# Performance work log

Hardware: AMD Instinct MI355X
Metric: run time of the kernel (lower is better)

Reference implementation:

```python
import jax, jax.numpy as jnp
import numpy as np

NUM_HEADS = 16
HEAD_SIZE = 64
MAX_POS = 2048  # config.max_position_embeddings


def setup_inputs() -> dict:
    key = jax.random.key(0)
    ks = jax.random.split(key, 8)
    B, Lq, Lk, D = 4, 1024, 2048, 1024
    s = 1.0 / np.sqrt(D)
    return {
        "hidden_states": jax.random.normal(ks[0], (B, Lk, D), jnp.float32),
        "query_hidden_states": jax.random.normal(ks[1], (B, Lq, D), jnp.float32),
        "attention_mask": jnp.zeros((B, 1, 1, Lk), jnp.float32),
        "Wq": jax.random.normal(ks[2], (D, D), jnp.float32) * s,
        "bq": jnp.zeros((D,), jnp.float32),
        "Wk": jax.random.normal(ks[3], (D, D), jnp.float32) * s,
        "bk": jnp.zeros((D,), jnp.float32),
        "Wv": jax.random.normal(ks[4], (D, D), jnp.float32) * s,
        "bv": jnp.zeros((D,), jnp.float32),
        "dist_emb": jax.random.normal(ks[5], (2 * MAX_POS - 1, HEAD_SIZE), jnp.float32) * 0.02,
    }


def _split_heads(x):
    # [B, L, H*Dh] -> [B, H, L, Dh]
    B, L, _ = x.shape
    return x.reshape(B, L, NUM_HEADS, HEAD_SIZE).transpose(0, 2, 1, 3)


def reference(hidden_states, query_hidden_states, attention_mask, Wq, bq, Wk, bk, Wv, bv, dist_emb):
    # Linear projections (torch Linear: x @ W.T + b)
    q = _split_heads(query_hidden_states @ Wq.T + bq)   # [B,H,Lq,Dh]
    k = _split_heads(hidden_states @ Wk.T + bk)          # [B,H,Lk,Dh]
    v = _split_heads(hidden_states @ Wv.T + bv)          # [B,H,Lk,Dh]

    scores = jnp.einsum('bhld,bhrd->bhlr', q, k)         # [B,H,Lq,Lk]

    # relative_key_query positional scores
    Lq, Lk = q.shape[2], k.shape[2]
    distance = jnp.arange(Lq)[:, None] - jnp.arange(Lk)[None, :]
    pe = dist_emb[distance + MAX_POS - 1]                # [Lq,Lk,Dh]
    scores = scores + jnp.einsum('bhld,lrd->bhlr', q, pe) + jnp.einsum('bhrd,lrd->bhlr', k, pe)

    scores = scores / np.sqrt(HEAD_SIZE) + attention_mask
    probs = jax.nn.softmax(scores, axis=-1)              # dropout p=0 (eval)
    ctx = jnp.einsum('bhlr,bhrd->bhld', probs, v)        # [B,H,Lq,Dh]
    B = ctx.shape[0]
    return ctx.transpose(0, 2, 1, 3).reshape(B, Lq, NUM_HEADS * HEAD_SIZE)
```

## Files before the change

### kernel.cpp

```cpp
#include <hip/hip_runtime.h>
#include <hip/hip_bf16.h>

#define B_   4
#define H_   16
#define LQ   1024
#define LK   2048
#define D_   1024
#define DH   64

typedef __attribute__((ext_vector_type(8))) short  short8;
typedef __attribute__((ext_vector_type(4))) float  float4_;
typedef __attribute__((ext_vector_type(4))) unsigned int uint4_;

static __device__ __forceinline__ float bf2f(unsigned short u) {
    unsigned int x = ((unsigned int)u) << 16;
    return __builtin_bit_cast(float, x);
}
static __device__ __forceinline__ unsigned short f2bf(float f) {
    unsigned int x = __builtin_bit_cast(unsigned int, f);
    unsigned int lsb = (x >> 16) & 1u;
    x += 0x7fffu + lsb;
    return (unsigned short)(x >> 16);
}
static __device__ __forceinline__ unsigned int pack2(float a, float b) {
    __hip_bfloat162 h = __float22bfloat162_rn(make_float2(a, b));
    unsigned int r;
    __builtin_memcpy(&r, &h, 4);
    return r;
}

#define MFMA(a, b, c) __builtin_amdgcn_mfma_f32_16x16x32_bf16((a), (b), (c), 0, 0, 0)

#define GLOAD_LDS16(g, l) __builtin_amdgcn_global_load_lds( \
    (const __attribute__((address_space(1))) unsigned int*)(const void*)(g), \
    (__attribute__((address_space(3))) unsigned int*)(void*)(l), 16, 0, 0)

__global__ __launch_bounds__(256) void conv_kernel(
    const float* __restrict__ Wq, const float* __restrict__ Wk,
    const float* __restrict__ Wv, const float* __restrict__ Eg,
    const float* __restrict__ Xq, const float* __restrict__ Xk,
    unsigned short* __restrict__ cWq, unsigned short* __restrict__ cWk,
    unsigned short* __restrict__ cWv, unsigned short* __restrict__ cEb,
    unsigned short* __restrict__ cXq, unsigned short* __restrict__ cXk)
{
    int bid = blockIdx.x;
    const float* src; unsigned short* dst; int nch;
    if (bid < 512)       { src = Wq; dst = cWq;              nch = 131072;  }
    else if (bid < 1024) { src = Wk; dst = cWk; bid -= 512;  nch = 131072;  }
    else if (bid < 1536) { src = Wv; dst = cWv; bid -= 1024; nch = 131072;  }
    else if (bid < 1664) { src = Eg; dst = cEb; bid -= 1536; nch = 32760;   }
    else if (bid < 3712) { src = Xq; dst = cXq; bid -= 1664; nch = 524288;  }
    else                 { src = Xk; dst = cXk; bid -= 3712; nch = 1048576; }
    int ch = bid * 256 + threadIdx.x;
    if (ch >= nch) return;
    const float* s = src + (size_t)ch * 8;
    float4_ v0 = *(const float4_*)s, v1 = *(const float4_*)(s + 4);
    uint4_ o;
    o[0] = pack2(v0[0], v0[1]); o[1] = pack2(v0[2], v0[3]);
    o[2] = pack2(v1[0], v1[1]); o[3] = pack2(v1[2], v1[3]);
    *(uint4_*)(dst + (size_t)ch * 8) = o;
}

__global__ __launch_bounds__(256) void proj_kernel(
    const unsigned short* __restrict__ Xq, const unsigned short* __restrict__ Xk,
    const unsigned short* __restrict__ Wq, const float* __restrict__ bq,
    const unsigned short* __restrict__ Wk, const float* __restrict__ bk,
    const unsigned short* __restrict__ Wv, const float* __restrict__ bv,
    unsigned short* __restrict__ Qh, unsigned short* __restrict__ Kh,
    unsigned short* __restrict__ VT)
{
    __shared__ short smem[32768];
    short* A0 = smem;
    short* B0 = smem + 8192;
    short* A1 = smem + 16384;
    short* B1 = smem + 24576;
    short* Cs = smem;

    int bid = blockIdx.x;
    int which, tm, tn;
    const unsigned short *X; const float* bias; const unsigned short* W;
    if (bid < 256)      { which = 0; int t = bid;       tm = t >> 3; tn = t & 7; X = Xq; W = Wq; bias = bq; }
    else if (bid < 768) { which = 1; int t = bid - 256; tm = t >> 3; tn = t & 7; X = Xk; W = Wk; bias = bk; }
    else                { which = 2; int t = bid - 768; tm = t >> 3; tn = t & 7; X = Xk; W = Wv; bias = bv; }

    int tid  = threadIdx.x;
    int wave = tid >> 6, lane = tid & 63;
    int wr = (wave >> 1) * 64, wc = (wave & 1) * 64;
    int m0 = tm * 128, n0 = tn * 128;

    float4_ acc[4][4];
    for (int a = 0; a < 4; ++a) for (int c = 0; c < 4; ++c) acc[a][c] = (float4_)0.0f;

    int rl = lane >> 3;
    int chs = (lane & 7) ^ rl;
    const unsigned short* Asrc = X + (size_t)(m0 + wave * 32 + rl) * D_ + (chs << 3);
    const unsigned short* Bsrc = W + (size_t)(n0 + wave * 32 + rl) * D_ + (chs << 3);

    int lrow = lane & 15, lk8 = (lane >> 4) * 8;
    int swz = lane & 7;

    auto stage = [&](short* Ad, short* Bd, int kt) {
        int k0 = kt * 64;
        #pragma unroll
        for (int c = 0; c < 4; ++c) {
            GLOAD_LDS16(Asrc + (size_t)(c * 8) * D_ + k0, &Ad[(wave * 32 + c * 8) * 64]);
            GLOAD_LDS16(Bsrc + (size_t)(c * 8) * D_ + k0, &Bd[(wave * 32 + c * 8) * 64]);
        }
    };
    auto compute = [&](const short* Aa, const short* Bb) {
        #pragma unroll
        for (int kk = 0; kk < 64; kk += 32) {
            int cgrp = (kk + lk8) >> 3;
            int coff = ((cgrp ^ swz) << 3);
            short8 af[4], bfr[4];
            #pragma unroll
            for (int rt = 0; rt < 4; ++rt)
                af[rt]  = *(const short8*)(&Aa[(wr + rt * 16 + lrow) * 64 + coff]);
            #pragma unroll
            for (int ct = 0; ct < 4; ++ct)
                bfr[ct] = *(const short8*)(&Bb[(wc + ct * 16 + lrow) * 64 + coff]);
            #pragma unroll
            for (int rt = 0; rt < 4; ++rt)
                #pragma unroll
                for (int ct = 0; ct < 4; ++ct)
                    acc[rt][ct] = MFMA(af[rt], bfr[ct], acc[rt][ct]);
        }
    };

    stage(A0, B0, 0);
    __syncthreads();
    for (int kt = 0; kt < 16; kt += 2) {
        if (kt + 1 < 16) stage(A1, B1, kt + 1);
        compute(A0, B0);
        __syncthreads();
        if (kt + 2 < 16) stage(A0, B0, kt + 2);
        compute(A1, B1);
        __syncthreads();
    }

    int lrow4 = (lane >> 4) * 4, lcol = lane & 15;
    if (which < 2) {
        int lsh = (which == 0) ? 10 : 11;
        int Lm1 = (1 << lsh) - 1;
        unsigned short* dst = (which == 0) ? Qh : Kh;
        for (int rt = 0; rt < 4; ++rt)
            for (int ct = 0; ct < 4; ++ct)
                for (int i = 0; i < 4; ++i) {
                    int m = m0 + wr + rt * 16 + lrow4 + i;
                    int n = n0 + wc + ct * 16 + lcol;
                    float v = acc[rt][ct][i] + bias[n];
                    int b = m >> lsh, s = m & Lm1;
                    int h = n >> 6, d = n & 63;
                    dst[((size_t)((b * H_ + h) << lsh) + (size_t)s) * DH + d] = f2bf(v);
                }
    } else {
        for (int rt = 0; rt < 4; ++rt)
            for (int ct = 0; ct < 4; ++ct)
                for (int i = 0; i < 4; ++i) {
                    int rl2 = wr + rt * 16 + lrow4 + i;
                    int cl  = wc + ct * 16 + lcol;
                    float v = acc[rt][ct][i] + bias[n0 + cl];
                    Cs[cl * 136 + rl2] = (short)f2bf(v);
                }
        __syncthreads();
        int b = m0 >> 11, r0 = m0 & 2047;
        int c = tid >> 1, half = tid & 1;
        int n = n0 + c, h = n >> 6, d = n & 63;
        unsigned short* dstp = VT + ((size_t)(b * H_ + h) * DH + d) * LK + r0 + half * 64;
        for (int j = 0; j < 8; ++j) {
            uint4_ v = *(const uint4_*)(&Cs[c * 136 + half * 64 + j * 8]);
            *(uint4_*)(dstp + j * 8) = v;
        }
    }
}

__global__ __launch_bounds__(256, 2) void attn_kernel(
    const unsigned short* __restrict__ Qh, const unsigned short* __restrict__ Kh,
    const unsigned short* __restrict__ VT, const unsigned short* __restrict__ Eb,
    const float* __restrict__ mask, float* __restrict__ out)
{
    __shared__ short smem[31360];
    short* Qs  = smem;
    short* Ks  = smem;
    short* VTs = smem + 4608;
    short* Es  = smem + 9216;
    short* Ps  = smem + 18432;
    unsigned int* Gqk = (unsigned int*)(smem + 23040);
    short* Gs  = smem + 23040;

    int bid = blockIdx.x;
    int l0 = (bid & 15) * 64;
    int bh = bid >> 4;
    int b  = bh >> 4, h = bh & 15;
    int tid = threadIdx.x, wave = tid >> 6, lane = tid & 63;
    int lr = lane & 15, lk8 = (lane >> 4) * 8, lr4 = (lane >> 4) * 4;

    for (int i = 0; i < 2; ++i) {
        int idx = tid + 256 * i, row = idx >> 3, g = (idx & 7) * 8;
        *(uint4_*)(&Qs[row * 72 + g]) =
            *(const uint4_*)(Qh + ((size_t)(bh * LQ + l0 + row)) * DH + g);
    }
    __syncthreads();
    short8 aq0 = *(const short8*)(&Qs[(wave * 16 + lr) * 72 + lk8]);
    short8 aq1 = *(const short8*)(&Qs[(wave * 16 + lr) * 72 + 32 + lk8]);

    float m_i[4], l_i[4];
    float4_ Oacc[4];
    for (int i = 0; i < 4; ++i) { m_i[i] = -1e30f; l_i[i] = 0.f; Oacc[i] = (float4_)0.f; }

    const unsigned short* Kbase = Kh + (size_t)bh * LK * DH;
    const unsigned short* Vbase = VT + (size_t)bh * DH * LK;

    int srow = tid >> 3;
    int sg   = (tid & 7) * 8;

    uint4_ kr0, kr1, vr0, vr1, er0, er1, er2, er3;
    auto load_tiles = [&](int it2) {
        int r0_ = it2 * 64, jb_ = l0 - r0_ + 1984;
        kr0 = *(const uint4_*)(Kbase + (size_t)(r0_ + srow) * DH + sg);
        kr1 = *(const uint4_*)(Kbase + (size_t)(r0_ + srow + 32) * DH + sg);
        vr0 = *(const uint4_*)(Vbase + (size_t)srow * LK + r0_ + sg);
        vr1 = *(const uint4_*)(Vbase + (size_t)(srow + 32) * LK + r0_ + sg);
        er0 = *(const uint4_*)(Eb + (size_t)(jb_ + srow) * DH + sg);
        er1 = *(const uint4_*)(Eb + (size_t)(jb_ + srow + 32) * DH + sg);
        er2 = *(const uint4_*)(Eb + (size_t)(jb_ + srow + 64) * DH + sg);
        er3 = *(const uint4_*)(Eb + (size_t)(jb_ + srow + 96) * DH + sg);
    };
    load_tiles(0);

    for (int it = 0; it < 32; ++it) {
        int r0 = it * 64;

        __syncthreads();
        *(uint4_*)(&Ks[srow * 72 + sg])         = kr0;
        *(uint4_*)(&Ks[(srow + 32) * 72 + sg])  = kr1;
        *(uint4_*)(&VTs[srow * 72 + sg])        = vr0;
        *(uint4_*)(&VTs[(srow + 32) * 72 + sg]) = vr1;
        *(uint4_*)(&Es[srow * 72 + sg])         = er0;
        *(uint4_*)(&Es[(srow + 32) * 72 + sg])  = er1;
        *(uint4_*)(&Es[(srow + 64) * 72 + sg])  = er2;
        *(uint4_*)(&Es[(srow + 96) * 72 + sg])  = er3;
        __syncthreads();
        if (it < 31) load_tiles(it + 1);

        float4_ Sacc[4];
        for (int c = 0; c < 4; ++c) {
            short8 b0 = *(const short8*)(&Ks[(c * 16 + lr) * 72 + lk8]);
            short8 b1 = *(const short8*)(&Ks[(c * 16 + lr) * 72 + 32 + lk8]);
            float4_ s = (float4_)0.f;
            s = MFMA(aq0, b0, s);
            s = MFMA(aq1, b1, s);
            Sacc[c] = s;
        }

        short8 ak0 = *(const short8*)(&Ks[(wave * 16 + lr) * 72 + lk8]);
        short8 ak1 = *(const short8*)(&Ks[(wave * 16 + lr) * 72 + 32 + lk8]);
        unsigned int gqp[5][2], gkp[5][2];
        for (int tt = 0; tt < 5; ++tt) {
            int tqi = wave + tt;
            short8 e0 = *(const short8*)(&Es[(tqi * 16 + lr) * 72 + lk8]);
            short8 e1 = *(const short8*)(&Es[(tqi * 16 + lr) * 72 + 32 + lk8]);
            float4_ g = (float4_)0.f;
            g = MFMA(aq0, e0, g); g = MFMA(aq1, e1, g);
            gqp[tt][0] = pack2(g[0], g[1]); gqp[tt][1] = pack2(g[2], g[3]);
            int tk = (3 - wave) + tt;
            short8 f0 = *(const short8*)(&Es[(tk * 16 + lr) * 72 + lk8]);
            short8 f1 = *(const short8*)(&Es[(tk * 16 + lr) * 72 + 32 + lk8]);
            float4_ gg = (float4_)0.f;
            gg = MFMA(ak0, f0, gg); gg = MFMA(ak1, f1, gg);
            gkp[tt][0] = pack2(gg[0], gg[1]); gkp[tt][1] = pack2(gg[2], gg[3]);
        }

        for (int tt = 0; tt < 5; ++tt) {
            int uq = (wave + tt) * 16 + lr;
            int uk = (3 - wave + tt) * 16 + lr;
            for (int i = 0; i < 4; ++i) {
                int row = wave * 16 + lr4 + i;
                unsigned int wq32 = gqp[tt][i >> 1], wk32 = gkp[tt][i >> 1];
                unsigned short vq = (unsigned short)((i & 1) ? (wq32 >> 16) : (wq32 & 0xffff));
                unsigned short vk = (unsigned short)((i & 1) ? (wk32 >> 16) : (wk32 & 0xffff));
                int tr = row - uq + 63;
                if ((unsigned)tr < 64u)
                    Gs[(row * 65 + tr) * 2] = (short)vq;
                int tl = uk + row - 63;
                if ((unsigned)tl < 64u)
                    Gs[(tl * 65 + row) * 2 + 1] = (short)vk;
            }
        }
        __syncthreads();

        float mk[4];
        for (int c = 0; c < 4; ++c) mk[c] = mask[b * LK + r0 + c * 16 + lr];
        for (int i = 0; i < 4; ++i) {
            int tl = wave * 16 + lr4 + i;
            const unsigned int* gr = Gqk + tl * 65 + lr;
            unsigned int gva[4];
            gva[0] = gr[0]; gva[1] = gr[16]; gva[2] = gr[32]; gva[3] = gr[48];
            float scv[4], mx = -1e30f;
            #pragma unroll
            for (int c = 0; c < 4; ++c) {
                float sq = bf2f((unsigned short)(gva[c] & 0xffff));
                float sk = bf2f((unsigned short)(gva[c] >> 16));
                float sc = (Sacc[c][i] + sq + sk) * 0.125f + mk[c];
                scv[c] = sc;
                mx = fmaxf(mx, sc);
            }
            for (int off = 1; off < 16; off <<= 1) mx = fmaxf(mx, __shfl_xor(mx, off, 64));
            float mnew = fmaxf(m_i[i], mx);
            float alpha = __expf(m_i[i] - mnew);
            m_i[i] = mnew;
            float e0 = __expf(scv[0] - mnew), e1 = __expf(scv[1] - mnew);
            float e2 = __expf(scv[2] - mnew), e3 = __expf(scv[3] - mnew);
            unsigned int p01 = pack2(e0, e1), p23 = pack2(e2, e3);
            float rs = bf2f((unsigned short)(p01 & 0xffff)) + bf2f((unsigned short)(p01 >> 16))
                     + bf2f((unsigned short)(p23 & 0xffff)) + bf2f((unsigned short)(p23 >> 16));
            for (int off = 1; off < 16; off <<= 1) rs += __shfl_xor(rs, off, 64);
            l_i[i] = l_i[i] * alpha + rs;
            for (int nt = 0; nt < 4; ++nt) Oacc[nt][i] *= alpha;
            short* Pr = Ps + tl * 72;
            Pr[ 0 + lr] = (short)(unsigned short)(p01 & 0xffff);
            Pr[16 + lr] = (short)(unsigned short)(p01 >> 16);
            Pr[32 + lr] = (short)(unsigned short)(p23 & 0xffff);
            Pr[48 + lr] = (short)(unsigned short)(p23 >> 16);
        }
        const short* Pa = Ps + (wave * 16 + lr) * 72;
        short8 ap0 = *(const short8*)(Pa + lk8);
        short8 ap1 = *(const short8*)(Pa + 32 + lk8);
        for (int nt = 0; nt < 4; ++nt) {
            short8 v0 = *(const short8*)(&VTs[(nt * 16 + lr) * 72 + lk8]);
            short8 v1 = *(const short8*)(&VTs[(nt * 16 + lr) * 72 + 32 + lk8]);
            Oacc[nt] = MFMA(ap0, v0, Oacc[nt]);
            Oacc[nt] = MFMA(ap1, v1, Oacc[nt]);
        }
    }

    for (int nt = 0; nt < 4; ++nt)
        for (int i = 0; i < 4; ++i) {
            int row = l0 + wave * 16 + lr4 + i;
            int col = h * 64 + nt * 16 + lr;
            out[(size_t)(b * LQ + row) * D_ + col] = Oacc[nt][i] / l_i[i];
        }
}

extern "C" void kernel_launch(void* const* d_in, const int* in_sizes, int n_in,
                              void* d_out, int out_size, void* d_ws, size_t ws_size,
                              hipStream_t stream) {
    (void)in_sizes; (void)n_in; (void)out_size; (void)ws_size;
    const float* Xk   = (const float*)d_in[0];
    const float* Xq   = (const float*)d_in[1];
    const float* mask = (const float*)d_in[2];
    const float* Wq   = (const float*)d_in[3];
    const float* bq   = (const float*)d_in[4];
    const float* Wk   = (const float*)d_in[5];
    const float* bk   = (const float*)d_in[6];
    const float* Wv   = (const float*)d_in[7];
    const float* bv   = (const float*)d_in[8];
    const float* Eg   = (const float*)d_in[9];

    unsigned short* Qh  = (unsigned short*)d_ws;
    unsigned short* Kh  = Qh  + (size_t)4194304;
    unsigned short* VT  = Kh  + (size_t)8388608;
    unsigned short* cWq = VT  + (size_t)8388608;
    unsigned short* cWk = cWq + (size_t)1048576;
    unsigned short* cWv = cWk + (size_t)1048576;
    unsigned short* cEb = cWv + (size_t)1048576;
    unsigned short* cXq = cEb + (size_t)262144;
    unsigned short* cXk = (unsigned short*)d_out;
    float* o = (float*)d_out;

    conv_kernel<<<7808, 256, 0, stream>>>(Wq, Wk, Wv, Eg, Xq, Xk,
                                          cWq, cWk, cWv, cEb, cXq, cXk);
    proj_kernel<<<1280, 256, 0, stream>>>(cXq, cXk, cWq, bq, cWk, bk, cWv, bv, Qh, Kh, VT);
    attn_kernel<<<1024, 256, 0, stream>>>(Qh, Kh, VT, cEb, mask, o);
}
```

Baseline: 425.3 us.

## Keep sliding positional-embedding window in registers and use DPP row reductions

The attention loop no longer stages the 128-row distance-embedding window through shared memory each iteration. Each lane holds the 8 E fragments in registers, and only the 4 newly needed tiles are loaded per step, using an xor-indexed double buffer across a two-iteration unrolled loop. The per-wave E MFMAs are restructured to skip tiles a wave does not need, and the K fragment is reused from the score loop. The 16-lane max and sum reductions switch from shfl_xor to DPP moves. Shared memory use drops, at the cost of many more VGPRs and strided direct global loads for E.

```diff
diff --git a/kernel.cpp b/kernel.cpp
--- a/kernel.cpp
+++ b/kernel.cpp
@@ -27,6 +27,12 @@
     unsigned int r;
     __builtin_memcpy(&r, &h, 4);
     return r;
+}
+template<int CTRL>
+static __device__ __forceinline__ float dppmv(float x) {
+    int i = __builtin_bit_cast(int, x);
+    int r = __builtin_amdgcn_update_dpp(i, i, CTRL, 0xf, 0xf, false);
+    return __builtin_bit_cast(float, r);
 }
 
 #define MFMA(a, b, c) __builtin_amdgcn_mfma_f32_16x16x32_bf16((a), (b), (c), 0, 0, 0)
@@ -179,14 +185,13 @@
     const unsigned short* __restrict__ VT, const unsigned short* __restrict__ Eb,
     const float* __restrict__ mask, float* __restrict__ out)
 {
-    __shared__ short smem[31360];
+    __shared__ short smem[22144];
     short* Qs  = smem;
     short* Ks  = smem;
     short* VTs = smem + 4608;
-    short* Es  = smem + 9216;
-    short* Ps  = smem + 18432;
-    unsigned int* Gqk = (unsigned int*)(smem + 23040);
-    short* Gs  = smem + 23040;
+    short* Ps  = smem + 9216;
+    unsigned int* Gqk = (unsigned int*)(smem + 13824);
+    short* Gs  = smem + 13824;
 
     int bid = blockIdx.x;
     int l0 = (bid & 15) * 64;
@@ -214,21 +219,31 @@
     int srow = tid >> 3;
     int sg   = (tid & 7) * 8;
 
-    uint4_ kr0, kr1, vr0, vr1, er0, er1, er2, er3;
-    auto load_tiles = [&](int it2) {
-        int r0_ = it2 * 64, jb_ = l0 - r0_ + 1984;
+    uint4_ kr0, kr1, vr0, vr1;
+    auto load_kv = [&](int nit) {
+        int r0_ = nit * 64;
         kr0 = *(const uint4_*)(Kbase + (size_t)(r0_ + srow) * DH + sg);
         kr1 = *(const uint4_*)(Kbase + (size_t)(r0_ + srow + 32) * DH + sg);
         vr0 = *(const uint4_*)(Vbase + (size_t)srow * LK + r0_ + sg);
         vr1 = *(const uint4_*)(Vbase + (size_t)(srow + 32) * LK + r0_ + sg);
-        er0 = *(const uint4_*)(Eb + (size_t)(jb_ + srow) * DH + sg);
-        er1 = *(const uint4_*)(Eb + (size_t)(jb_ + srow + 32) * DH + sg);
-        er2 = *(const uint4_*)(Eb + (size_t)(jb_ + srow + 64) * DH + sg);
-        er3 = *(const uint4_*)(Eb + (size_t)(jb_ + srow + 96) * DH + sg);
     };
-    load_tiles(0);
-
-    for (int it = 0; it < 32; ++it) {
+    load_kv(0);
+
+    short8 ef[8][2];
+    {
+        const unsigned short* ep = Eb + (size_t)(l0 + 1984 + lr) * DH + lk8;
+        #pragma unroll
+        for (int t = 0; t < 8; ++t) {
+            ef[t][0] = *(const short8*)(ep + (size_t)t * 16 * DH);
+            ef[t][1] = *(const short8*)(ep + (size_t)t * 16 * DH + 32);
+        }
+    }
+
+    for (int it2 = 0; it2 < 32; it2 += 2) {
+      #pragma unroll
+      for (int sub = 0; sub < 2; ++sub) {
+        const int it = it2 + sub;
+        const int p4 = sub * 4;
         int r0 = it * 64;
 
         __syncthreads();
@@ -236,14 +251,12 @@
         *(uint4_*)(&Ks[(srow + 32) * 72 + sg])  = kr1;
         *(uint4_*)(&VTs[srow * 72 + sg])        = vr0;
         *(uint4_*)(&VTs[(srow + 32) * 72 + sg]) = vr1;
-        *(uint4_*)(&Es[srow * 72 + sg])         = er0;
-        *(uint4_*)(&Es[(srow + 32) * 72 + sg])  = er1;
-        *(uint4_*)(&Es[(srow + 64) * 72 + sg])  = er2;
-        *(uint4_*)(&Es[(srow + 96) * 72 + sg])  = er3;
-        __syncthreads();
-        if (it < 31) load_tiles(it + 1);
-
+        __syncthreads();
+        if (it < 31) load_kv(it + 1);
+
+        short8 ak0, ak1;
         float4_ Sacc[4];
+        #pragma unroll
         for (int c = 0; c < 4; ++c) {
             short8 b0 = *(const short8*)(&Ks[(c * 16 + lr) * 72 + lk8]);
             short8 b1 = *(const short8*)(&Ks[(c * 16 + lr) * 72 + 32 + lk8]);
@@ -251,46 +264,60 @@
             s = MFMA(aq0, b0, s);
             s = MFMA(aq1, b1, s);
             Sacc[c] = s;
-        }
-
-        short8 ak0 = *(const short8*)(&Ks[(wave * 16 + lr) * 72 + lk8]);
-        short8 ak1 = *(const short8*)(&Ks[(wave * 16 + lr) * 72 + 32 + lk8]);
-        unsigned int gqp[5][2], gkp[5][2];
-        for (int tt = 0; tt < 5; ++tt) {
-            int tqi = wave + tt;
-            short8 e0 = *(const short8*)(&Es[(tqi * 16 + lr) * 72 + lk8]);
-            short8 e1 = *(const short8*)(&Es[(tqi * 16 + lr) * 72 + 32 + lk8]);
-            float4_ g = (float4_)0.f;
-            g = MFMA(aq0, e0, g); g = MFMA(aq1, e1, g);
-            gqp[tt][0] = pack2(g[0], g[1]); gqp[tt][1] = pack2(g[2], g[3]);
-            int tk = (3 - wave) + tt;
-            short8 f0 = *(const short8*)(&Es[(tk * 16 + lr) * 72 + lk8]);
-            short8 f1 = *(const short8*)(&Es[(tk * 16 + lr) * 72 + 32 + lk8]);
-            float4_ gg = (float4_)0.f;
-            gg = MFMA(ak0, f0, gg); gg = MFMA(ak1, f1, gg);
-            gkp[tt][0] = pack2(gg[0], gg[1]); gkp[tt][1] = pack2(gg[2], gg[3]);
-        }
-
-        for (int tt = 0; tt < 5; ++tt) {
-            int uq = (wave + tt) * 16 + lr;
-            int uk = (3 - wave + tt) * 16 + lr;
-            for (int i = 0; i < 4; ++i) {
-                int row = wave * 16 + lr4 + i;
-                unsigned int wq32 = gqp[tt][i >> 1], wk32 = gkp[tt][i >> 1];
-                unsigned short vq = (unsigned short)((i & 1) ? (wq32 >> 16) : (wq32 & 0xffff));
-                unsigned short vk = (unsigned short)((i & 1) ? (wk32 >> 16) : (wk32 & 0xffff));
-                int tr = row - uq + 63;
-                if ((unsigned)tr < 64u)
-                    Gs[(row * 65 + tr) * 2] = (short)vq;
-                int tl = uk + row - 63;
-                if ((unsigned)tl < 64u)
-                    Gs[(tl * 65 + row) * 2 + 1] = (short)vk;
+            if (c == 0 || c == wave) { ak0 = b0; ak1 = b1; }
+        }
+
+        #pragma unroll
+        for (int t = 0; t < 8; ++t) {
+            int dq = t - wave, dk = t - 3 + wave;
+            bool needq = (unsigned)dq < 5u, needk = (unsigned)dk < 5u;
+            if (!(needq || needk)) continue;
+            short8 e0 = ef[t ^ p4][0], e1 = ef[t ^ p4][1];
+            int u = t * 16 + lr;
+            if (needq) {
+                float4_ g = (float4_)0.f;
+                g = MFMA(aq0, e0, g); g = MFMA(aq1, e1, g);
+                unsigned int p0 = pack2(g[0], g[1]), p1 = pack2(g[2], g[3]);
+                #pragma unroll
+                for (int i = 0; i < 4; ++i) {
+                    int row = wave * 16 + lr4 + i;
+                    unsigned int w32 = (i >> 1) ? p1 : p0;
+                    unsigned short vq = (unsigned short)((i & 1) ? (w32 >> 16) : (w32 & 0xffff));
+                    int tr = row - u + 63;
+                    if ((unsigned)tr < 64u)
+                        Gs[(row * 65 + tr) * 2] = (short)vq;
+                }
             }
-        }
-        __syncthreads();
+            if (needk) {
+                float4_ gg = (float4_)0.f;
+                gg = MFMA(ak0, e0, gg); gg = MFMA(ak1, e1, gg);
+                unsigned int q0 = pack2(gg[0], gg[1]), q1 = pack2(gg[2], gg[3]);
+                #pragma unroll
+                for (int i = 0; i < 4; ++i) {
+                    int row = wave * 16 + lr4 + i;
+                    unsigned int w32 = (i >> 1) ? q1 : q0;
+                    unsigned short vk = (unsigned short)((i & 1) ? (w32 >> 16) : (w32 & 0xffff));
+                    int tl = u + row - 63;
+                    if ((unsigned)tl < 64u)
+                        Gs[(tl * 65 + row) * 2 + 1] = (short)vk;
+                }
+            }
+        }
+        __syncthreads();
+
+        if (it < 31) {
+            const unsigned short* ep =
+                Eb + (size_t)(l0 + 1984 - 64 * (it + 1) + lr) * DH + lk8;
+            #pragma unroll
+            for (int t = 0; t < 4; ++t) {
+                ef[t ^ p4 ^ 4][0] = *(const short8*)(ep + (size_t)t * 16 * DH);
+                ef[t ^ p4 ^ 4][1] = *(const short8*)(ep + (size_t)t * 16 * DH + 32);
+            }
+        }
 
         float mk[4];
         for (int c = 0; c < 4; ++c) mk[c] = mask[b * LK + r0 + c * 16 + lr];
+        #pragma unroll
         for (int i = 0; i < 4; ++i) {
             int tl = wave * 16 + lr4 + i;
             const unsigned int* gr = Gqk + tl * 65 + lr;
@@ -305,7 +332,10 @@
                 scv[c] = sc;
                 mx = fmaxf(mx, sc);
             }
-            for (int off = 1; off < 16; off <<= 1) mx = fmaxf(mx, __shfl_xor(mx, off, 64));
+            mx = fmaxf(mx, dppmv<0xB1>(mx));
+            mx = fmaxf(mx, dppmv<0x4E>(mx));
+            mx = fmaxf(mx, dppmv<0x141>(mx));
+            mx = fmaxf(mx, dppmv<0x140>(mx));
             float mnew = fmaxf(m_i[i], mx);
             float alpha = __expf(m_i[i] - mnew);
             m_i[i] = mnew;
@@ -314,7 +344,10 @@
             unsigned int p01 = pack2(e0, e1), p23 = pack2(e2, e3);
             float rs = bf2f((unsigned short)(p01 & 0xffff)) + bf2f((unsigned short)(p01 >> 16))
                      + bf2f((unsigned short)(p23 & 0xffff)) + bf2f((unsigned short)(p23 >> 16));
-            for (int off = 1; off < 16; off <<= 1) rs += __shfl_xor(rs, off, 64);
+            rs += dppmv<0xB1>(rs);
+            rs += dppmv<0x4E>(rs);
+            rs += dppmv<0x141>(rs);
+            rs += dppmv<0x140>(rs);
             l_i[i] = l_i[i] * alpha + rs;
             for (int nt = 0; nt < 4; ++nt) Oacc[nt][i] *= alpha;
             short* Pr = Ps + tl * 72;
@@ -326,12 +359,14 @@
         const short* Pa = Ps + (wave * 16 + lr) * 72;
         short8 ap0 = *(const short8*)(Pa + lk8);
         short8 ap1 = *(const short8*)(Pa + 32 + lk8);
+        #pragma unroll
         for (int nt = 0; nt < 4; ++nt) {
             short8 v0 = *(const short8*)(&VTs[(nt * 16 + lr) * 72 + lk8]);
             short8 v1 = *(const short8*)(&VTs[(nt * 16 + lr) * 72 + 32 + lk8]);
             Oacc[nt] = MFMA(ap0, v0, Oacc[nt]);
             Oacc[nt] = MFMA(ap1, v1, Oacc[nt]);
         }
+      }
     }
 
     for (int nt = 0; nt < 4; ++nt)
```

Measured after the change: 443.3 us. +4.3%, slower.
